# Kernel tuning notes

Hardware: AMD Instinct MI355X
Metric: run time of the kernel (lower is better)

The kernel has to match this reference:

```python
import jax, jax.numpy as jnp
import numpy as np

QBITS = 8
QP = float(2 ** (QBITS - 1) - 1)  # 127 for 8-bit symmetric quantization


def quant(x, K):
    # learned-scale symmetric uniform quantization (fake-quant / dequant),
    # straight-through estimator for gradients
    xc = jnp.clip(x / K, -1.0, 1.0)
    q = jnp.round(xc * QP) / QP
    return (xc + jax.lax.stop_gradient(q - xc)) * K


def setup_inputs() -> dict:
    key = jax.random.key(0)
    k0, k1, k2 = jax.random.split(key, 3)
    B, S, D, H = 64, 197, 768, 3072  # ViT-B/16: 197 tokens, d=768, mlp=3072
    hidden_state = jax.random.normal(k0, (B, S, D), jnp.float32)
    # xavier-uniform-like scale for weights
    W1 = jax.random.normal(k1, (H, D), jnp.float32) * np.float32(1.0 / np.sqrt(D))
    b1 = jnp.zeros((H,), jnp.float32)
    W2 = jax.random.normal(k2, (D, H), jnp.float32) * np.float32(1.0 / np.sqrt(H))
    b2 = jnp.zeros((D,), jnp.float32)
    # learned per-layer activation / weight scale factors (kmlp_* lists)
    ka1 = jnp.array([3.0], jnp.float32)
    kw1 = jnp.array([0.1], jnp.float32)
    ka2 = jnp.array([3.0], jnp.float32)
    kw2 = jnp.array([0.1], jnp.float32)
    return {"hidden_state": hidden_state, "W1": W1, "b1": b1, "W2": W2,
            "b2": b2, "ka1": ka1, "kw1": kw1, "ka2": ka2, "kw2": kw2}


def reference(hidden_state, W1, b1, W2, b2, ka1, kw1, ka2, kw2):
    # fc1: quantize activations with Ka, weights with Kw, then GEMM + bias
    h = jnp.einsum("bsd,hd->bsh", quant(hidden_state, ka1), quant(W1, kw1)) + b1
    h = jax.nn.gelu(h, approximate=False)  # F.gelu default = exact erf
    # dropout is identity in eval mode
    out = jnp.einsum("bsh,dh->bsd", quant(h, ka2), quant(W2, kw2)) + b2
    return out
```

## Files before the change

kernel.cpp:

```cpp
#include <hip/hip_runtime.h>
#include <stdint.h>


typedef __attribute__((ext_vector_type(4))) int i32x4;

static constexpr int MROWS = 12608;
static constexpr int MPAD  = 12672;
static constexpr int DDIM  = 768;
static constexpr int HDIM  = 3072;

__device__ __forceinline__ int quant_one(float x, float K) {
    float xc = x / K;
    xc = fminf(fmaxf(xc, -1.0f), 1.0f);
    return (int)rintf(xc * 127.0f);
}

__global__ void quant_fused_kernel(const float* __restrict__ x,
                                   const float* __restrict__ w1,
                                   const float* __restrict__ w2,
                                   int8_t* __restrict__ a8,
                                   int8_t* __restrict__ w1q,
                                   int8_t* __restrict__ w2q,
                                   const float* __restrict__ ka1,
                                   const float* __restrict__ kw1,
                                   const float* __restrict__ kw2) {
    constexpr int G1 = MPAD * DDIM / 4;
    constexpr int GV = MROWS * DDIM / 4;
    constexpr int G2 = HDIM * DDIM / 4;
    int i = blockIdx.x * 256 + threadIdx.x;
    const float4* src; int* dst; float K; int idx; bool valid = true;
    if (i < G1) {
        idx = i;           src = (const float4*)x;  dst = (int*)a8;  K = ka1[0];
        valid = i < GV;
    } else if (i < G1 + G2) {
        idx = i - G1;      src = (const float4*)w1; dst = (int*)w1q; K = kw1[0];
    } else if (i < G1 + 2 * G2) {
        idx = i - G1 - G2; src = (const float4*)w2; dst = (int*)w2q; K = kw2[0];
    } else return;
    int packed = 0;
    if (valid) {
        float4 v = src[idx];
        packed = (quant_one(v.x, K) & 255)
               | ((quant_one(v.y, K) & 255) << 8)
               | ((quant_one(v.z, K) & 255) << 16)
               | ((quant_one(v.w, K) & 255) << 24);
    }
    dst[idx] = packed;
}

__device__ __forceinline__ void load16_to_lds(const int8_t* g, const int8_t* l) {
    __builtin_amdgcn_global_load_lds(
        (const __attribute__((address_space(1))) void*)g,
        (__attribute__((address_space(3))) void*)l, 16, 0, 0);
}

template<int KD, int ND, bool EPI1>
__global__ __launch_bounds__(256, 3)
void gemm_i8_kernel(const int8_t* __restrict__ A, const int8_t* __restrict__ B,
                    int8_t* __restrict__ qout, float* __restrict__ fout,
                    const float* __restrict__ bias,
                    const float* __restrict__ kA, const float* __restrict__ kW,
                    const float* __restrict__ kQ) {
    __shared__ __align__(16) int8_t As0[128 * 64];
    __shared__ __align__(16) int8_t Bs0[128 * 64];
    __shared__ __align__(16) int8_t As1[128 * 64];
    __shared__ __align__(16) int8_t Bs1[128 * 64];

    const int tid  = threadIdx.x;
    const int lane = tid & 63;
    const int wave = tid >> 6;
    const int wr   = wave >> 1;
    const int wc   = wave & 1;

    constexpr int NXB = ND / 128;
    const int nwg = gridDim.x;
    const int q   = nwg >> 3, r = nwg & 7;
    const int xcd = blockIdx.x & 7, loc = blockIdx.x >> 3;
    const int nb  = (xcd < r ? xcd * (q + 1) : r * (q + 1) + (xcd - r) * q) + loc;
    const int bm  = (nb / NXB) * 128;
    const int bn  = (nb % NXB) * 128;

    i32x4 acc[4][4] = {};

    const int srow = tid >> 2;
    const int soff = (((tid & 3) ^ ((tid >> 3) & 3)) << 4);
    const int8_t* gA = A + (size_t)(bm + srow) * KD + soff;
    const int8_t* gB = B + (size_t)(bn + srow) * KD + soff;
    const int ldst = tid * 16;

#define STAGE(LA, LB, ktb)                                                     \
    do {                                                                       \
        const int8_t* a_ = gA + (ktb);                                         \
        const int8_t* b_ = gB + (ktb);                                         \
        load16_to_lds(a_,                   LA + ldst);                        \
        load16_to_lds(a_ + (size_t)64 * KD, LA + 4096 + ldst);                 \
        load16_to_lds(b_,                   LB + ldst);                        \
        load16_to_lds(b_ + (size_t)64 * KD, LB + 4096 + ldst);                 \
    } while (0)

    const int fr = lane & 15;
    const int q4 = lane >> 4;
    const int cs = ((q4 ^ ((fr >> 1) & 3)) << 4);
    int aoff[4], boff[4];
#pragma unroll
    for (int m = 0; m < 4; ++m) aoff[m] = (wr * 64 + m * 16 + fr) * 64 + cs;
#pragma unroll
    for (int n = 0; n < 4; ++n) boff[n] = (wc * 64 + n * 16 + fr) * 64 + cs;

#define COMPUTE(LA, LB)                                                        \
    do {                                                                       \
        i32x4 af[4], bf[4];                                                    \
        _Pragma("unroll")                                                      \
        for (int m = 0; m < 4; ++m)                                            \
            af[m] = *reinterpret_cast<const i32x4*>(LA + aoff[m]);             \
        _Pragma("unroll")                                                      \
        for (int n = 0; n < 4; ++n)                                            \
            bf[n] = *reinterpret_cast<const i32x4*>(LB + boff[n]);             \
        __builtin_amdgcn_s_setprio(1);                                         \
        _Pragma("unroll")                                                      \
        for (int m = 0; m < 4; ++m)                                            \
            _Pragma("unroll")                                                  \
            for (int n = 0; n < 4; ++n)                                        \
                acc[m][n] = __builtin_amdgcn_mfma_i32_16x16x64_i8(             \
                    af[m], bf[n], acc[m][n], 0, 0, 0);                         \
        __builtin_amdgcn_s_setprio(0);                                         \
    } while (0)

    constexpr int NT = KD / 64;
    STAGE(As0, Bs0, 0);
    __syncthreads();

    for (int t = 0; t < NT; t += 2) {
        STAGE(As1, Bs1, (t + 1) * 64);
        COMPUTE(As0, Bs0);
        __syncthreads();
        if (t + 2 < NT) STAGE(As0, Bs0, (t + 2) * 64);
        COMPUTE(As1, Bs1);
        __syncthreads();
    }
#undef STAGE
#undef COMPUTE

    const float sAW = kA[0] * kW[0] * (1.0f / 16129.0f);
    float kq = 1.0f;
    if constexpr (EPI1) kq = kQ[0];

    const int row0 = bm + wr * 64 + (q4 << 2);
    const int col0 = bn + wc * 64 + fr;
#pragma unroll
    for (int m = 0; m < 4; ++m) {
#pragma unroll
        for (int n = 0; n < 4; ++n) {
            const int col = col0 + n * 16;
            const float bv = bias[col];
#pragma unroll
            for (int j = 0; j < 4; ++j) {
                const int row = row0 + m * 16 + j;
                float h = (float)acc[m][n][j] * sAW + bv;
                if constexpr (EPI1) {
                    float g  = 0.5f * h * (1.0f + erff(h * 0.70710678118654752f));
                    float xc = fminf(fmaxf(g / kq, -1.0f), 1.0f);
                    qout[(size_t)row * ND + col] = (int8_t)(int)rintf(xc * 127.0f);
                } else {
                    if (row < MROWS)
                        fout[(size_t)row * ND + col] = h;
                }
            }
        }
    }
}

extern "C" void kernel_launch(void* const* d_in, const int* in_sizes, int n_in,
                              void* d_out, int out_size, void* d_ws, size_t ws_size,
                              hipStream_t stream) {
    const float* hidden = (const float*)d_in[0];
    const float* W1     = (const float*)d_in[1];
    const float* b1     = (const float*)d_in[2];
    const float* W2     = (const float*)d_in[3];
    const float* b2     = (const float*)d_in[4];
    const float* ka1    = (const float*)d_in[5];
    const float* kw1    = (const float*)d_in[6];
    const float* ka2    = (const float*)d_in[7];
    const float* kw2    = (const float*)d_in[8];
    float* out = (float*)d_out;

    int8_t* a8  = (int8_t*)d_ws;
    int8_t* w1q = a8  + (size_t)MPAD * DDIM;
    int8_t* w2q = w1q + (size_t)HDIM * DDIM;
    int8_t* h8  = w2q + (size_t)DDIM * HDIM;

    {
        constexpr int GTOT = (MPAD * DDIM + 2 * HDIM * DDIM) / 4;
        quant_fused_kernel<<<(GTOT + 255) / 256, 256, 0, stream>>>(
            hidden, W1, W2, a8, w1q, w2q, ka1, kw1, kw2);
    }

    gemm_i8_kernel<DDIM, HDIM, true>
        <<<(HDIM / 128) * (MPAD / 128), 256, 0, stream>>>
        (a8, w1q, h8, nullptr, b1, ka1, kw1, ka2);

    gemm_i8_kernel<HDIM, DDIM, false>
        <<<(DDIM / 128) * (MPAD / 128), 256, 0, stream>>>
        (h8, w2q, nullptr, out, b2, ka2, kw2, nullptr);
}
```

Before: 225.4 us.

## Switch int8 GEMMs to 256x256 tiles with 8 waves and phased K=128 pipeline

Replaces the 128x128, 4-wave int8 MFMA GEMM with a 256x256-tile, 512-thread kernel. Each K step is now 128 bytes, double-buffered in 128 KB of LDS. Global-to-LDS loads are split into quarter chunks interleaved with compute phases separated by raw s_barrier, and B fragments are reused across two M halves. The aim is more arithmetic intensity per byte of global and LDS traffic. The cost is heavy register pressure (32 accumulators), fewer workgroups, and the last M tile being clamped so it overlaps and recomputes rows.

```diff
diff --git a/kernel.cpp b/kernel.cpp
--- a/kernel.cpp
+++ b/kernel.cpp
@@ -54,109 +54,125 @@
         (__attribute__((address_space(3))) void*)l, 16, 0, 0);
 }
 
+#define BAR()    asm volatile("s_barrier" ::: "memory")
+#define VMCNT0() asm volatile("s_waitcnt vmcnt(0)" ::: "memory")
+
 template<int KD, int ND, bool EPI1>
-__global__ __launch_bounds__(256, 3)
-void gemm_i8_kernel(const int8_t* __restrict__ A, const int8_t* __restrict__ B,
-                    int8_t* __restrict__ qout, float* __restrict__ fout,
-                    const float* __restrict__ bias,
-                    const float* __restrict__ kA, const float* __restrict__ kW,
-                    const float* __restrict__ kQ) {
-    __shared__ __align__(16) int8_t As0[128 * 64];
-    __shared__ __align__(16) int8_t Bs0[128 * 64];
-    __shared__ __align__(16) int8_t As1[128 * 64];
-    __shared__ __align__(16) int8_t Bs1[128 * 64];
+__global__ __launch_bounds__(512, 2)
+void gemm_i8_256(const int8_t* __restrict__ A, const int8_t* __restrict__ B,
+                 int8_t* __restrict__ qout, float* __restrict__ fout,
+                 const float* __restrict__ bias,
+                 const float* __restrict__ kA, const float* __restrict__ kW,
+                 const float* __restrict__ kQ) {
+    __shared__ __align__(16) int8_t Ab0[32768];
+    __shared__ __align__(16) int8_t Bb0[32768];
+    __shared__ __align__(16) int8_t Ab1[32768];
+    __shared__ __align__(16) int8_t Bb1[32768];
 
     const int tid  = threadIdx.x;
     const int lane = tid & 63;
     const int wave = tid >> 6;
-    const int wr   = wave >> 1;
-    const int wc   = wave & 1;
-
-    constexpr int NXB = ND / 128;
+    const int wr   = wave >> 2;
+    const int wc   = wave & 3;
+
+    constexpr int NXB = ND / 256;
     const int nwg = gridDim.x;
     const int q   = nwg >> 3, r = nwg & 7;
     const int xcd = blockIdx.x & 7, loc = blockIdx.x >> 3;
     const int nb  = (xcd < r ? xcd * (q + 1) : r * (q + 1) + (xcd - r) * q) + loc;
-    const int bm  = (nb / NXB) * 128;
-    const int bn  = (nb % NXB) * 128;
-
-    i32x4 acc[4][4] = {};
-
-    const int srow = tid >> 2;
-    const int soff = (((tid & 3) ^ ((tid >> 3) & 3)) << 4);
-    const int8_t* gA = A + (size_t)(bm + srow) * KD + soff;
-    const int8_t* gB = B + (size_t)(bn + srow) * KD + soff;
-    const int ldst = tid * 16;
-
-#define STAGE(LA, LB, ktb)                                                     \
+    const int bm  = min((nb / NXB) * 256, MPAD - 256);
+    const int bn  = (nb % NXB) * 256;
+
+    i32x4 acc[8][4] = {};
+    i32x4 bf_[4];
+
+    const int soff = (((tid & 7) ^ ((tid >> 3) & 7)) << 4);
+    const int8_t* gA = A + (size_t)(bm + (tid >> 3)) * KD + soff;
+    const int8_t* gB = B + (size_t)(bn + (tid >> 3)) * KD + soff;
+
+#define STG(GP, LB, KB, H)                                                     \
     do {                                                                       \
-        const int8_t* a_ = gA + (ktb);                                         \
-        const int8_t* b_ = gB + (ktb);                                         \
-        load16_to_lds(a_,                   LA + ldst);                        \
-        load16_to_lds(a_ + (size_t)64 * KD, LA + 4096 + ldst);                 \
-        load16_to_lds(b_,                   LB + ldst);                        \
-        load16_to_lds(b_ + (size_t)64 * KD, LB + 4096 + ldst);                 \
+        load16_to_lds(GP + (size_t)((H) * 128) * KD + (KB),                    \
+                      LB + (H) * 16384 + 16 * tid);                            \
+        load16_to_lds(GP + (size_t)((H) * 128 + 64) * KD + (KB),               \
+                      LB + (H) * 16384 + 8192 + 16 * tid);                     \
     } while (0)
 
-    const int fr = lane & 15;
-    const int q4 = lane >> 4;
-    const int cs = ((q4 ^ ((fr >> 1) & 3)) << 4);
-    int aoff[4], boff[4];
-#pragma unroll
-    for (int m = 0; m < 4; ++m) aoff[m] = (wr * 64 + m * 16 + fr) * 64 + cs;
-#pragma unroll
-    for (int n = 0; n < 4; ++n) boff[n] = (wc * 64 + n * 16 + fr) * 64 + cs;
-
-#define COMPUTE(LA, LB)                                                        \
+    const int fr  = lane & 15;
+    const int q4  = lane >> 4;
+    const int sl0 = ((q4 ^ (fr & 7)) << 4);
+    int aoff[8], boff[4];
+#pragma unroll
+    for (int m = 0; m < 8; ++m) aoff[m] = (wr * 128 + m * 16 + fr) * 128 + sl0;
+#pragma unroll
+    for (int n = 0; n < 4; ++n) boff[n] = (wc * 64 + n * 16 + fr) * 128 + sl0;
+
+#define PHASE(MH, KS, ABUF, BBUF, READB, ...)                                  \
     do {                                                                       \
-        i32x4 af[4], bf[4];                                                    \
+        i32x4 af_[4];                                                          \
+        if (READB) {                                                           \
+            _Pragma("unroll")                                                  \
+            for (int n = 0; n < 4; ++n)                                        \
+                bf_[n] = *reinterpret_cast<const i32x4*>(                      \
+                    BBUF + (boff[n] ^ ((KS) * 64)));                           \
+        }                                                                      \
         _Pragma("unroll")                                                      \
         for (int m = 0; m < 4; ++m)                                            \
-            af[m] = *reinterpret_cast<const i32x4*>(LA + aoff[m]);             \
-        _Pragma("unroll")                                                      \
-        for (int n = 0; n < 4; ++n)                                            \
-            bf[n] = *reinterpret_cast<const i32x4*>(LB + boff[n]);             \
+            af_[m] = *reinterpret_cast<const i32x4*>(                          \
+                ABUF + (aoff[(MH) * 4 + m] ^ ((KS) * 64)));                    \
+        __VA_ARGS__;                                                           \
+        BAR();                                                                 \
         __builtin_amdgcn_s_setprio(1);                                         \
         _Pragma("unroll")                                                      \
         for (int m = 0; m < 4; ++m)                                            \
             _Pragma("unroll")                                                  \
             for (int n = 0; n < 4; ++n)                                        \
-                acc[m][n] = __builtin_amdgcn_mfma_i32_16x16x64_i8(             \
-                    af[m], bf[n], acc[m][n], 0, 0, 0);                         \
+                acc[(MH) * 4 + m][n] = __builtin_amdgcn_mfma_i32_16x16x64_i8(  \
+                    af_[m], bf_[n], acc[(MH) * 4 + m][n], 0, 0, 0);            \
         __builtin_amdgcn_s_setprio(0);                                         \
+        BAR();                                                                 \
     } while (0)
 
-    constexpr int NT = KD / 64;
-    STAGE(As0, Bs0, 0);
-    __syncthreads();
-
-    for (int t = 0; t < NT; t += 2) {
-        STAGE(As1, Bs1, (t + 1) * 64);
-        COMPUTE(As0, Bs0);
-        __syncthreads();
-        if (t + 2 < NT) STAGE(As0, Bs0, (t + 2) * 64);
-        COMPUTE(As1, Bs1);
-        __syncthreads();
-    }
-#undef STAGE
-#undef COMPUTE
+    constexpr int NIT = KD / 256;
+
+    STG(gA, Ab0, 0, 0); STG(gA, Ab0, 0, 1);
+    STG(gB, Bb0, 0, 0); STG(gB, Bb0, 0, 1);
+    VMCNT0(); BAR();
+
+    for (int j = 0; j < NIT; ++j) {
+        const int kb1 = j * 256 + 128;
+        const int kb2 = j * 256 + 256;
+        const bool more = (j + 1 < NIT);
+        PHASE(0, 0, Ab0, Bb0, true,  STG(gA, Ab1, kb1, 0));
+        PHASE(1, 0, Ab0, Bb0, false, STG(gA, Ab1, kb1, 1));
+        PHASE(0, 1, Ab0, Bb0, true,  STG(gB, Bb1, kb1, 0));
+        PHASE(1, 1, Ab0, Bb0, false, STG(gB, Bb1, kb1, 1));
+        VMCNT0(); BAR();
+        PHASE(0, 0, Ab1, Bb1, true,  if (more) STG(gA, Ab0, kb2, 0));
+        PHASE(1, 0, Ab1, Bb1, false, if (more) STG(gA, Ab0, kb2, 1));
+        PHASE(0, 1, Ab1, Bb1, true,  if (more) STG(gB, Bb0, kb2, 0));
+        PHASE(1, 1, Ab1, Bb1, false, if (more) STG(gB, Bb0, kb2, 1));
+        VMCNT0(); BAR();
+    }
+#undef PHASE
+#undef STG
 
     const float sAW = kA[0] * kW[0] * (1.0f / 16129.0f);
     float kq = 1.0f;
     if constexpr (EPI1) kq = kQ[0];
 
-    const int row0 = bm + wr * 64 + (q4 << 2);
+    const int row0 = bm + wr * 128 + (q4 << 2);
     const int col0 = bn + wc * 64 + fr;
 #pragma unroll
-    for (int m = 0; m < 4; ++m) {
+    for (int m = 0; m < 8; ++m) {
 #pragma unroll
         for (int n = 0; n < 4; ++n) {
             const int col = col0 + n * 16;
             const float bv = bias[col];
 #pragma unroll
-            for (int j = 0; j < 4; ++j) {
-                const int row = row0 + m * 16 + j;
-                float h = (float)acc[m][n][j] * sAW + bv;
+            for (int jj = 0; jj < 4; ++jj) {
+                const int row = row0 + m * 16 + jj;
+                float h = (float)acc[m][n][jj] * sAW + bv;
                 if constexpr (EPI1) {
                     float g  = 0.5f * h * (1.0f + erff(h * 0.70710678118654752f));
                     float xc = fminf(fmaxf(g / kq, -1.0f), 1.0f);
@@ -195,11 +211,11 @@
             hidden, W1, W2, a8, w1q, w2q, ka1, kw1, kw2);
     }
 
-    gemm_i8_kernel<DDIM, HDIM, true>
-        <<<(HDIM / 128) * (MPAD / 128), 256, 0, stream>>>
+    gemm_i8_256<DDIM, HDIM, true>
+        <<<((MPAD + 255) / 256) * (HDIM / 256), 512, 0, stream>>>
         (a8, w1q, h8, nullptr, b1, ka1, kw1, ka2);
 
-    gemm_i8_kernel<HDIM, DDIM, false>
-        <<<(DDIM / 128) * (MPAD / 128), 256, 0, stream>>>
+    gemm_i8_256<HDIM, DDIM, false>
+        <<<((MPAD + 255) / 256) * (DDIM / 256), 512, 0, stream>>>
         (h8, w2q, nullptr, out, b2, ka2, kw2, nullptr);
 }
```

Measured after the change: 345.4 us. +53.2%, slower.
